# Optimization experiments

Measured on AMD Instinct MI355X. Metric: run time of the kernel, lower is better.

Reference implementation:

```python
import jax, jax.numpy as jnp
import numpy as np

N_NODES = 100000
D = 256
HIDDEN = 256
E = 262144


def setup_inputs() -> dict:
    key = jax.random.key(0)
    ks = jax.random.split(key, 8)
    x_src = jax.random.normal(ks[0], (N_NODES, D), dtype=jnp.float32)
    x_dst = jax.random.normal(ks[1], (N_NODES, D), dtype=jnp.float32)
    # MLP params: Linear(in_src+in_dst -> hidden), ReLU, Linear(hidden -> 1)
    W1 = jax.random.normal(ks[2], (2 * D, HIDDEN), dtype=jnp.float32) * (1.0 / np.sqrt(2 * D))
    b1 = jnp.zeros((HIDDEN,), dtype=jnp.float32)
    W2 = jax.random.normal(ks[3], (HIDDEN, 1), dtype=jnp.float32) * (1.0 / np.sqrt(HIDDEN))
    b2 = jnp.zeros((1,), dtype=jnp.float32)
    edge_index = jax.random.randint(ks[4], (2, E), 0, N_NODES, dtype=jnp.int64)
    neg_edge_index = jax.random.randint(ks[5], (2, E), 0, N_NODES, dtype=jnp.int64)
    return {"x_src": x_src, "x_dst": x_dst, "W1": W1, "b1": b1, "W2": W2,
            "b2": b2, "edge_index": edge_index, "neg_edge_index": neg_edge_index}


def _score(xs, xd, W1, b1, W2, b2):
    # MLP scorer: cat -> Linear -> ReLU -> Linear -> squeeze
    h = jnp.concatenate([xs, xd], axis=-1) @ W1 + b1   # [E, HIDDEN]
    h = jax.nn.relu(h)
    return (h @ W2 + b2).squeeze(-1)                   # [E]


def reference(x_src, x_dst, W1, b1, W2, b2, edge_index, neg_edge_index):
    src, dst = edge_index[0], edge_index[1]
    nsrc, ndst = neg_edge_index[0], neg_edge_index[1]
    pos = _score(x_src[src], x_dst[dst], W1, b1, W2, b2)
    neg = _score(x_src[nsrc], x_dst[ndst], W1, b1, W2, b2)
    return pos, neg
```

## Files before the change

kernel.cpp:

```cpp
#include <hip/hip_runtime.h>

#define D_IN   256
#define HID    256
#define NNODES 100000
#define NEDGE  262144

typedef short short8            __attribute__((ext_vector_type(8)));
typedef float float4v           __attribute__((ext_vector_type(4)));
typedef unsigned short ushort8  __attribute__((ext_vector_type(8)));

__device__ __forceinline__ unsigned short f32_to_bf16_rne(float f) {
    unsigned int u = __float_as_uint(f);
    unsigned int r = u + 0x7FFFu + ((u >> 16) & 1u);
    return (unsigned short)(r >> 16);
}
__device__ __forceinline__ float bf16_to_f32(unsigned short h) {
    return __uint_as_float(((unsigned int)h) << 16);
}

__global__ __launch_bounds__(256) void convert_w(
    const float* __restrict__ W1, unsigned short* __restrict__ Wt)
{
    __shared__ float tile[64][65];
    const int z = blockIdx.z, kb = blockIdx.x * 64, nb = blockIdx.y * 64;
    const int t = threadIdx.x;
    const int g = t >> 6, c = t & 63;
#pragma unroll
    for (int r = 0; r < 16; r++) {
        int kl = g * 16 + r;
        tile[kl][c] = W1[((size_t)(z * 256 + kb + kl)) * 256 + nb + c];
    }
    __syncthreads();
#pragma unroll
    for (int r = 0; r < 16; r++) {
        int nl = g * 16 + r;
        Wt[((size_t)(z * 256 + nb + nl)) * 256 + kb + c] = f32_to_bf16_rne(tile[c][nl]);
    }
}

#define SA 72

__global__ __launch_bounds__(512) void gemm_xw_mfma(
    const float* __restrict__ Xsrc, const float* __restrict__ Xdst,
    const unsigned short* __restrict__ Wt, const float* __restrict__ b1,
    unsigned short* __restrict__ U, unsigned short* __restrict__ V)
{
    const int zz = blockIdx.z;
    const float* X = zz ? Xdst : Xsrc;
    const unsigned short* Wz = Wt + (size_t)zz * 256 * 256;
    unsigned short* C = zz ? V : U;

    const int m0 = blockIdx.x * 128;

    __shared__ __align__(16) unsigned short smem[27648];
    unsigned short* As = smem;
    unsigned short* Bs = smem + 9216;

    const int t = threadIdx.x;
    const int w = t >> 6, lane = t & 63;
    const int wm = w >> 2, wn = w & 3;
    const int quad = lane >> 4, l16 = lane & 15;

    float4v acc[4][4];
#pragma unroll
    for (int mi = 0; mi < 4; mi++)
#pragma unroll
        for (int ni = 0; ni < 4; ni++) acc[mi][ni] = (float4v){0.f, 0.f, 0.f, 0.f};

    for (int ks = 0; ks < D_IN; ks += 64) {
#pragma unroll
        for (int i = 0; i < 4; i++) {
            int s = t + i * 512;
            int row = s >> 4, c4 = (s & 15) << 2;
            int gr = m0 + row; if (gr >= NNODES) gr = NNODES - 1;
            float4 a = *(const float4*)(X + (size_t)gr * D_IN + ks + c4);
            ushort4 p;
            p.x = f32_to_bf16_rne(a.x); p.y = f32_to_bf16_rne(a.y);
            p.z = f32_to_bf16_rne(a.z); p.w = f32_to_bf16_rne(a.w);
            *(ushort4*)(As + row * SA + c4) = p;
        }
#pragma unroll
        for (int i = 0; i < 4; i++) {
            int s = t + i * 512;
            int n = s >> 3, seg = s & 7;
            *(int4*)(Bs + n * SA + seg * 8) =
                *(const int4*)(Wz + (size_t)n * 256 + ks + seg * 8);
        }
        __syncthreads();
#pragma unroll
        for (int kk = 0; kk < 64; kk += 32) {
            short8 af[4], bf[4];
#pragma unroll
            for (int mi = 0; mi < 4; mi++)
                af[mi] = *(const short8*)(As + (wm * 64 + mi * 16 + l16) * SA + kk + quad * 8);
#pragma unroll
            for (int ni = 0; ni < 4; ni++)
                bf[ni] = *(const short8*)(Bs + (wn * 64 + ni * 16 + l16) * SA + kk + quad * 8);
#pragma unroll
            for (int mi = 0; mi < 4; mi++)
#pragma unroll
                for (int ni = 0; ni < 4; ni++)
                    acc[mi][ni] = __builtin_amdgcn_mfma_f32_16x16x32_bf16(
                        af[mi], bf[ni], acc[mi][ni], 0, 0, 0);
        }
        __syncthreads();
    }

    float bias[4];
#pragma unroll
    for (int ni = 0; ni < 4; ni++)
        bias[ni] = (zz == 0) ? b1[wn * 64 + ni * 16 + l16] : 0.f;

    unsigned short* Cs = smem;
#pragma unroll
    for (int h = 0; h < 2; h++) {
        if ((wn >> 1) == h) {
#pragma unroll
            for (int mi = 0; mi < 4; mi++)
#pragma unroll
                for (int ni = 0; ni < 4; ni++) {
                    int cl = (wn & 1) * 64 + ni * 16 + l16;
#pragma unroll
                    for (int r = 0; r < 4; r++) {
                        int row = wm * 64 + mi * 16 + quad * 4 + r;
                        Cs[row * 136 + cl] = f32_to_bf16_rne(acc[mi][ni][r] + bias[ni]);
                    }
                }
        }
        __syncthreads();
#pragma unroll
        for (int i = 0; i < 4; i++) {
            int s = t + i * 512;
            int row = s >> 4, seg = s & 15;
            int gr = m0 + row;
            if (gr < NNODES)
                *(int4*)(C + (size_t)gr * HID + h * 128 + seg * 8) =
                    *(const int4*)(Cs + row * 136 + seg * 8);
        }
        __syncthreads();
    }
}

__global__ __launch_bounds__(256) void edge_score_bf16(
    const unsigned short* __restrict__ U, const unsigned short* __restrict__ V,
    const float* __restrict__ W2, const float* __restrict__ b2,
    const int* __restrict__ epos, const int* __restrict__ eneg,
    float* __restrict__ out)
{
    const int w = threadIdx.x >> 6, lane = threadIdx.x & 63;
    const int half = lane >> 5, hl = lane & 31;
    const int ebase = blockIdx.x * 64 + w * 16;

    const int* ei = (ebase < NEDGE) ? epos : eneg;
    const int eb2 = (ebase < NEDGE) ? ebase : ebase - NEDGE;

    int sidx[8], didx[8];
#pragma unroll
    for (int p = 0; p < 8; p++) {
        int e = eb2 + 2 * p + half;
        sidx[p] = ei[e];
        didx[p] = ei[NEDGE + e];
    }
    ushort8 uu[8], vv[8];
#pragma unroll
    for (int p = 0; p < 8; p++)
        uu[p] = *(const ushort8*)(U + (size_t)sidx[p] * HID + hl * 8);
#pragma unroll
    for (int p = 0; p < 8; p++)
        vv[p] = *(const ushort8*)(V + (size_t)didx[p] * HID + hl * 8);

    float w2r[8];
    *(float4*)&w2r[0] = *(const float4*)(W2 + hl * 8);
    *(float4*)&w2r[4] = *(const float4*)(W2 + hl * 8 + 4);
    const float bb2 = b2[0];

#pragma unroll
    for (int p = 0; p < 8; p++) {
        float s = 0.f;
#pragma unroll
        for (int q = 0; q < 8; q++)
            s += fmaxf(bf16_to_f32(uu[p][q]) + bf16_to_f32(vv[p][q]), 0.f) * w2r[q];
#pragma unroll
        for (int off = 16; off; off >>= 1)
            s += __shfl_xor(s, off, 64);
        if (hl == 0) out[ebase + 2 * p + half] = s + bb2;
    }
}

__global__ __launch_bounds__(256) void edge_score_direct(
    const float* __restrict__ xs_, const float* __restrict__ xd_,
    const float* __restrict__ W1, const float* __restrict__ b1,
    const float* __restrict__ W2, const float* __restrict__ b2,
    const int* __restrict__ epos, const int* __restrict__ eneg,
    float* __restrict__ out)
{
    __shared__ float xrow[2 * D_IN];
    __shared__ float red[256];
    const int e = blockIdx.x;
    const int* ei = (e < NEDGE) ? epos : eneg;
    const int e2  = (e < NEDGE) ? e : e - NEDGE;
    const int s = ei[e2];
    const int d = ei[NEDGE + e2];
    const int t = threadIdx.x;

    xrow[t]        = xs_[(size_t)s * D_IN + t];
    xrow[D_IN + t] = xd_[(size_t)d * D_IN + t];
    __syncthreads();

    float acc = b1[t];
    for (int k = 0; k < 2 * D_IN; k++)
        acc += xrow[k] * W1[(size_t)k * HID + t];
    acc = fmaxf(acc, 0.f);
    red[t] = acc * W2[t];
    __syncthreads();
    for (int st = 128; st; st >>= 1) {
        if (t < st) red[t] += red[t + st];
        __syncthreads();
    }
    if (t == 0) out[e] = red[0] + b2[0];
}

extern "C" void kernel_launch(void* const* d_in, const int* in_sizes, int n_in,
                              void* d_out, int out_size, void* d_ws, size_t ws_size,
                              hipStream_t stream) {
    const float* x_src = (const float*)d_in[0];
    const float* x_dst = (const float*)d_in[1];
    const float* W1    = (const float*)d_in[2];
    const float* b1    = (const float*)d_in[3];
    const float* W2    = (const float*)d_in[4];
    const float* b2    = (const float*)d_in[5];
    const int*   epos  = (const int*)d_in[6];
    const int*   eneg  = (const int*)d_in[7];
    float* out = (float*)d_out;

    const size_t uv   = (size_t)NNODES * HID;
    const size_t need = (2 * uv + 2 * 256 * 256) * sizeof(unsigned short);
    if (ws_size >= need) {
        unsigned short* U  = (unsigned short*)d_ws;
        unsigned short* V  = U + uv;
        unsigned short* Wt = V + uv;
        convert_w<<<dim3(4, 4, 2), 256, 0, stream>>>(W1, Wt);
        dim3 g1((NNODES + 127) / 128, 1, 2);
        gemm_xw_mfma<<<g1, 512, 0, stream>>>(x_src, x_dst, Wt, b1, U, V);
        edge_score_bf16<<<(2 * NEDGE) / 64, 256, 0, stream>>>(U, V, W2, b2, epos, eneg, out);
    } else {
        edge_score_direct<<<2 * NEDGE, 256, 0, stream>>>(x_src, x_dst, W1, b1, W2, b2, epos, eneg, out);
    }
}
```

Baseline: 334.3 us.

## Keep whole W1 half resident in LDS with persistent warps over row groups

The node GEMM now loads the full 256x256 bf16 weight slice into a 128 KB XOR-swizzled LDS buffer once per block. It runs 256 persistent 1024-thread blocks in which each wave computes a 16-row by 256-col output tile, streaming A straight from global memory into registers with a one-step prefetch. This removes the per-k-step A/B LDS staging, the barriers and the LDS-staged epilogue, at the cost of one block per CU and 64 accumulator vectors per lane. The swapped MFMA operands let each lane write its four outputs directly as ushort4.

```diff
diff --git a/kernel.cpp b/kernel.cpp
--- a/kernel.cpp
+++ b/kernel.cpp
@@ -4,6 +4,9 @@
 #define HID    256
 #define NNODES 100000
 #define NEDGE  262144
+#define NGROUPS 6250
+#define GBLK   128
+#define GW     16
 
 typedef short short8            __attribute__((ext_vector_type(8)));
 typedef float float4v           __attribute__((ext_vector_type(4)));
@@ -38,9 +41,7 @@
     }
 }
 
-#define SA 72
-
-__global__ __launch_bounds__(512) void gemm_xw_mfma(
+__global__ __launch_bounds__(1024, 4) void gemm_xw_mfma(
     const float* __restrict__ Xsrc, const float* __restrict__ Xdst,
     const unsigned short* __restrict__ Wt, const float* __restrict__ b1,
     unsigned short* __restrict__ U, unsigned short* __restrict__ V)
@@ -50,94 +51,77 @@
     const unsigned short* Wz = Wt + (size_t)zz * 256 * 256;
     unsigned short* C = zz ? V : U;
 
-    const int m0 = blockIdx.x * 128;
-
-    __shared__ __align__(16) unsigned short smem[27648];
-    unsigned short* As = smem;
-    unsigned short* Bs = smem + 9216;
+    __shared__ __align__(16) unsigned short Bs[256 * 256];
 
     const int t = threadIdx.x;
+#pragma unroll
+    for (int i = 0; i < 8; i++) {
+        int s = t + (i << 10);
+        int n = s >> 5, c = s & 31;
+        *(int4*)(Bs + n * 256 + ((c ^ (n & 7)) << 3)) =
+            *(const int4*)(Wz + (size_t)n * 256 + (c << 3));
+    }
+    __syncthreads();
+
     const int w = t >> 6, lane = t & 63;
-    const int wm = w >> 2, wn = w & 3;
     const int quad = lane >> 4, l16 = lane & 15;
-
-    float4v acc[4][4];
-#pragma unroll
-    for (int mi = 0; mi < 4; mi++)
-#pragma unroll
-        for (int ni = 0; ni < 4; ni++) acc[mi][ni] = (float4v){0.f, 0.f, 0.f, 0.f};
-
-    for (int ks = 0; ks < D_IN; ks += 64) {
-#pragma unroll
-        for (int i = 0; i < 4; i++) {
-            int s = t + i * 512;
-            int row = s >> 4, c4 = (s & 15) << 2;
-            int gr = m0 + row; if (gr >= NNODES) gr = NNODES - 1;
-            float4 a = *(const float4*)(X + (size_t)gr * D_IN + ks + c4);
-            ushort4 p;
-            p.x = f32_to_bf16_rne(a.x); p.y = f32_to_bf16_rne(a.y);
-            p.z = f32_to_bf16_rne(a.z); p.w = f32_to_bf16_rne(a.w);
-            *(ushort4*)(As + row * SA + c4) = p;
+    const int r7 = l16 & 7;
+    const unsigned short* Bl = Bs + l16 * 256;
+
+    const int wid = w * GBLK + blockIdx.x;
+
+    for (int g = wid; g < NGROUPS; g += GBLK * GW) {
+        const int row = (g << 4) + l16;
+        const float* Ap = X + (size_t)row * D_IN + (quad << 3);
+
+        float4v acc[16];
+#pragma unroll
+        for (int i = 0; i < 16; i++) acc[i] = (float4v){0.f, 0.f, 0.f, 0.f};
+
+        float4 a0 = *(const float4*)(Ap);
+        float4 a1 = *(const float4*)(Ap + 4);
+
+#pragma unroll 1
+        for (int kk = 0; kk < 8; kk++) {
+            float4 p0 = a0, p1 = a1;
+            if (kk < 7) {
+                p0 = *(const float4*)(Ap + (kk + 1) * 32);
+                p1 = *(const float4*)(Ap + (kk + 1) * 32 + 4);
+            }
+            short8 af;
+            af[0] = (short)f32_to_bf16_rne(a0.x);
+            af[1] = (short)f32_to_bf16_rne(a0.y);
+            af[2] = (short)f32_to_bf16_rne(a0.z);
+            af[3] = (short)f32_to_bf16_rne(a0.w);
+            af[4] = (short)f32_to_bf16_rne(a1.x);
+            af[5] = (short)f32_to_bf16_rne(a1.y);
+            af[6] = (short)f32_to_bf16_rne(a1.z);
+            af[7] = (short)f32_to_bf16_rne(a1.w);
+
+            const int cs = (((kk << 2) + quad) ^ r7) << 3;
+#pragma unroll
+            for (int tt = 0; tt < 16; tt++) {
+                short8 bf = *(const short8*)(Bl + tt * 4096 + cs);
+                acc[tt] = __builtin_amdgcn_mfma_f32_16x16x32_bf16(bf, af, acc[tt], 0, 0, 0);
+            }
+            a0 = p0; a1 = p1;
         }
-#pragma unroll
-        for (int i = 0; i < 4; i++) {
-            int s = t + i * 512;
-            int n = s >> 3, seg = s & 7;
-            *(int4*)(Bs + n * SA + seg * 8) =
-                *(const int4*)(Wz + (size_t)n * 256 + ks + seg * 8);
+
+        unsigned short* Crow = C + (size_t)row * HID + (quad << 2);
+#pragma unroll
+        for (int tt = 0; tt < 16; tt++) {
+            float4v a = acc[tt];
+            if (zz == 0) {
+                float4 bb = *(const float4*)(b1 + tt * 16 + (quad << 2));
+                a[0] += bb.x; a[1] += bb.y; a[2] += bb.z; a[3] += bb.w;
+            }
+            ushort4 pk;
+            pk.x = f32_to_bf16_rne(a[0]);
+            pk.y = f32_to_bf16_rne(a[1]);
+            pk.z = f32_to_bf16_rne(a[2]);
+            pk.w = f32_to_bf16_rne(a[3]);
+            *(ushort4*)(Crow + tt * 16) = pk;
         }
-        __syncthreads();
-#pragma unroll
-        for (int kk = 0; kk < 64; kk += 32) {
-            short8 af[4], bf[4];
-#pragma unroll
-            for (int mi = 0; mi < 4; mi++)
-                af[mi] = *(const short8*)(As + (wm * 64 + mi * 16 + l16) * SA + kk + quad * 8);
-#pragma unroll
-            for (int ni = 0; ni < 4; ni++)
-                bf[ni] = *(const short8*)(Bs + (wn * 64 + ni * 16 + l16) * SA + kk + quad * 8);
-#pragma unroll
-            for (int mi = 0; mi < 4; mi++)
-#pragma unroll
-                for (int ni = 0; ni < 4; ni++)
-                    acc[mi][ni] = __builtin_amdgcn_mfma_f32_16x16x32_bf16(
-                        af[mi], bf[ni], acc[mi][ni], 0, 0, 0);
-        }
-        __syncthreads();
-    }
-
-    float bias[4];
-#pragma unroll
-    for (int ni = 0; ni < 4; ni++)
-        bias[ni] = (zz == 0) ? b1[wn * 64 + ni * 16 + l16] : 0.f;
-
-    unsigned short* Cs = smem;
-#pragma unroll
-    for (int h = 0; h < 2; h++) {
-        if ((wn >> 1) == h) {
-#pragma unroll
-            for (int mi = 0; mi < 4; mi++)
-#pragma unroll
-                for (int ni = 0; ni < 4; ni++) {
-                    int cl = (wn & 1) * 64 + ni * 16 + l16;
-#pragma unroll
-                    for (int r = 0; r < 4; r++) {
-                        int row = wm * 64 + mi * 16 + quad * 4 + r;
-                        Cs[row * 136 + cl] = f32_to_bf16_rne(acc[mi][ni][r] + bias[ni]);
-                    }
-                }
-        }
-        __syncthreads();
-#pragma unroll
-        for (int i = 0; i < 4; i++) {
-            int s = t + i * 512;
-            int row = s >> 4, seg = s & 15;
-            int gr = m0 + row;
-            if (gr < NNODES)
-                *(int4*)(C + (size_t)gr * HID + h * 128 + seg * 8) =
-                    *(const int4*)(Cs + row * 136 + seg * 8);
-        }
-        __syncthreads();
     }
 }
 
@@ -240,8 +224,7 @@
         unsigned short* V  = U + uv;
         unsigned short* Wt = V + uv;
         convert_w<<<dim3(4, 4, 2), 256, 0, stream>>>(W1, Wt);
-        dim3 g1((NNODES + 127) / 128, 1, 2);
-        gemm_xw_mfma<<<g1, 512, 0, stream>>>(x_src, x_dst, Wt, b1, U, V);
+        gemm_xw_mfma<<<dim3(GBLK, 1, 2), 1024, 0, stream>>>(x_src, x_dst, Wt, b1, U, V);
         edge_score_bf16<<<(2 * NEDGE) / 64, 256, 0, stream>>>(U, V, W2, b2, epos, eneg, out);
     } else {
         edge_score_direct<<<2 * NEDGE, 256, 0, stream>>>(x_src, x_dst, W1, b1, W2, b2, epos, eneg, out);
```

Measured after the change: 326.4 us. 2.4% less time.
